# Performance work log

Hardware: AMD Instinct MI355X
Metric: run time of the kernel (lower is better)

## Reference

```python
import jax, jax.numpy as jnp
import numpy as np
import math
from jax import lax

B, T, D, K, H, MLP_DIM, WIN = 4, 2048, 1024, 64, 4, 4096, 128
KH = K // H          # eigenstates per head
HD = D // H          # attention head dim


def layer_norm(x, g, b, eps=1e-5):
    mu = jnp.mean(x, axis=-1, keepdims=True)
    var = jnp.mean(jnp.square(x - mu), axis=-1, keepdims=True)
    return (x - mu) * lax.rsqrt(var + eps) * g + b


def setup_inputs() -> dict:
    key = jax.random.key(0)
    ks = jax.random.split(key, 16)
    s = 0.02
    # layer_idx=1, n_layers=6 -> depth_ratio=0.2, decay_center=-1.7
    return {
        "x": jax.random.normal(ks[0], (B, T, D), jnp.float32),
        "prev_eigenstates": jax.random.normal(ks[1], (B, T, 2 * K), jnp.float32),
        "norm1_g": jnp.ones((D,), jnp.float32),
        "norm1_b": jnp.zeros((D,), jnp.float32),
        "in_proj_w": jax.random.normal(ks[2], (2 * K, D), jnp.float32) * s,
        "memory_gate": jnp.array(-3.0, jnp.float32),
        "memory_proj_w": jnp.eye(2 * K, dtype=jnp.float32),
        "log_decay": jax.random.uniform(ks[3], (K,), jnp.float32, -2.7, -1.2),
        "frequency": jnp.linspace(0.0, 2 * math.pi * (1 - 1 / K), K, dtype=jnp.float32),
        "coupling": jnp.tile(jnp.eye(KH, dtype=jnp.float32), (H, 1, 1))
                    + 0.01 * jax.random.normal(ks[4], (H, KH, KH), jnp.float32) / math.sqrt(KH),
        "main_gate_w": jax.random.normal(ks[5], (D, D), jnp.float32) * s,
        "main_gate_b": jnp.full((D,), -2.0, jnp.float32),
        "out_proj_w": jax.random.normal(ks[6], (D, 2 * K), jnp.float32) * s,
        "attn_norm_g": jnp.ones((D,), jnp.float32),
        "attn_norm_b": jnp.zeros((D,), jnp.float32),
        "attn_in_w": jax.random.normal(ks[7], (3 * D, D), jnp.float32) * s,
        "attn_in_b": jnp.zeros((3 * D,), jnp.float32),
        "attn_out_w": jax.random.normal(ks[8], (D, D), jnp.float32) * s,
        "attn_out_b": jnp.zeros((D,), jnp.float32),
        "norm2_g": jnp.ones((D,), jnp.float32),
        "norm2_b": jnp.zeros((D,), jnp.float32),
        "mlp_w1": jax.random.normal(ks[9], (MLP_DIM, D), jnp.float32) * s,
        "mlp_b1": jnp.zeros((MLP_DIM,), jnp.float32),
        "mlp_w2": jax.random.normal(ks[10], (D, MLP_DIM), jnp.float32) * s,
        "mlp_b2": jnp.zeros((D,), jnp.float32),
    }


def eigenstate_fft(log_decay, frequency, beta_r, beta_i):
    # diagonal complex SSM recurrence: c_t = lam * c_{t-1} + beta_t
    lam = jnp.exp(log_decay)
    lr = lam * jnp.cos(frequency)   # (K,)
    li = lam * jnp.sin(frequency)
    br = jnp.transpose(beta_r, (1, 0, 2))  # (T,B,K)
    bi = jnp.transpose(beta_i, (1, 0, 2))

    def step(carry, inp):
        sr, si = carry
        xr, xi = inp
        nr = lr * sr - li * si + xr
        ni = lr * si + li * sr + xi
        return (nr, ni), (nr, ni)

    init = (jnp.zeros(br.shape[1:], br.dtype), jnp.zeros(bi.shape[1:], bi.dtype))
    _, (cr, ci) = lax.scan(step, init, (br, bi))
    return jnp.transpose(cr, (1, 0, 2)), jnp.transpose(ci, (1, 0, 2))


def reference(x, prev_eigenstates, norm1_g, norm1_b, in_proj_w, memory_gate,
              memory_proj_w, log_decay, frequency, coupling, main_gate_w,
              main_gate_b, out_proj_w, attn_norm_g, attn_norm_b, attn_in_w,
              attn_in_b, attn_out_w, attn_out_b, norm2_g, norm2_b,
              mlp_w1, mlp_b1, mlp_w2, mlp_b2):
    b, t, d = x.shape
    residual = x
    x_norm = layer_norm(x, norm1_g, norm1_b)

    beta = jnp.einsum('btd,kd->btk', x_norm, in_proj_w)        # (B,T,2K)
    beta_r, beta_i = jnp.split(beta, 2, axis=-1)

    # cross-layer memory
    mg = jax.nn.sigmoid(memory_gate)
    prev = jnp.einsum('btk,jk->btj', prev_eigenstates, memory_proj_w)
    pr, pi = jnp.split(prev, 2, axis=-1)
    beta_r = beta_r + mg * pr
    beta_i = beta_i + mg * pi

    c_r, c_i = eigenstate_fft(log_decay, frequency, beta_r, beta_i)  # (B,T,K)

    # per-head coupling
    c_r_h = c_r.reshape(b, t, H, KH)
    c_i_h = c_i.reshape(b, t, H, KH)
    c_r = jnp.einsum('hjk,bthk->bthj', coupling, c_r_h).reshape(b, t, K)
    c_i = jnp.einsum('hjk,bthk->bthj', coupling, c_i_h).reshape(b, t, K)
    eigenstates_out = jnp.concatenate([c_r, c_i], axis=-1)     # (B,T,2K)

    h = jnp.einsum('btk,dk->btd', eigenstates_out, out_proj_w)
    # spectral gate (band gates computed in torch are unused in the output)
    main_g = jax.nn.sigmoid(jnp.einsum('btd,ed->bte', x_norm, main_gate_w) + main_gate_b)
    h = main_g * h
    x = residual + h

    # sliding-window attention (dense masked MHA, as in the source)
    attn_in = layer_norm(x, attn_norm_g, attn_norm_b)
    qkv = jnp.einsum('btd,ed->bte', attn_in, attn_in_w) + attn_in_b
    q, k_, v = jnp.split(qkv, 3, axis=-1)
    q = q.reshape(b, t, H, HD).transpose(0, 2, 1, 3)           # (B,H,T,hd)
    k_ = k_.reshape(b, t, H, HD).transpose(0, 2, 1, 3)
    v = v.reshape(b, t, H, HD).transpose(0, 2, 1, 3)
    scale = 1.0 / math.sqrt(HD)
    scores = jnp.einsum('bhqd,bhkd->bhqk', q, k_) * scale
    idx = jnp.arange(t)
    diff = idx[:, None] - idx[None, :]
    allowed = (diff >= 0) & (diff <= WIN)                      # True = attend
    scores = jnp.where(allowed, scores, jnp.finfo(scores.dtype).min)
    attn = jax.nn.softmax(scores, axis=-1)
    ao = jnp.einsum('bhqk,bhkd->bhqd', attn, v)
    ao = ao.transpose(0, 2, 1, 3).reshape(b, t, d)
    ao = jnp.einsum('btd,ed->bte', ao, attn_out_w) + attn_out_b
    x = x + ao

    # MLP
    x2 = layer_norm(x, norm2_g, norm2_b)
    m = jax.nn.silu(jnp.einsum('btd,md->btm', x2, mlp_w1) + mlp_b1)
    m = jnp.einsum('btm,dm->btd', m, mlp_w2) + mlp_b2
    x = x + m
    return (x, eigenstates_out)
```

## Files before the change

kernel.cpp:

```cpp
#include <hip/hip_runtime.h>


typedef __bf16 bf16_t;
typedef bf16_t bf16x8 __attribute__((ext_vector_type(8)));
typedef bf16_t bf16x4 __attribute__((ext_vector_type(4)));
typedef float  f32x4  __attribute__((ext_vector_type(4)));

#define Tc   2048
#define Dc   1024
#define BTc  8192
#define K2c  128
#define MLPc 4096

struct ConvSeg { const float* src; bf16_t* dst; int n; };
struct ConvArgs { ConvSeg s[9]; };

__global__ __launch_bounds__(256) void convert_kernel(ConvArgs a) {
    ConvSeg sg = a.s[blockIdx.y];
    int i = (blockIdx.x * 256 + threadIdx.x) * 4;
    if (i >= sg.n) return;
    float4 v = *(const float4*)(sg.src + i);
    bf16x4 o;
    o[0] = (bf16_t)v.x; o[1] = (bf16_t)v.y; o[2] = (bf16_t)v.z; o[3] = (bf16_t)v.w;
    *(bf16x4*)(sg.dst + i) = o;
}

__global__ __launch_bounds__(256) void ln_kernel(const float* __restrict__ x,
                                                 const float* __restrict__ g,
                                                 const float* __restrict__ bb,
                                                 bf16_t* __restrict__ out) {
    int row = blockIdx.x;
    int tid = threadIdx.x;
    float4 v = ((const float4*)(x + (size_t)row * Dc))[tid];
    float s  = v.x + v.y + v.z + v.w;
    float ss = v.x * v.x + v.y * v.y + v.z * v.z + v.w * v.w;
#pragma unroll
    for (int d = 32; d > 0; d >>= 1) {
        s  += __shfl_down(s, d);
        ss += __shfl_down(ss, d);
    }
    __shared__ float red[8];
    int wv = tid >> 6;
    if ((tid & 63) == 0) { red[wv] = s; red[4 + wv] = ss; }
    __syncthreads();
    s  = red[0] + red[1] + red[2] + red[3];
    ss = red[4] + red[5] + red[6] + red[7];
    float mean = s * (1.0f / Dc);
    float var  = ss * (1.0f / Dc) - mean * mean;
    float rstd = rsqrtf(var + 1e-5f);
    float4 g4 = ((const float4*)g)[tid];
    float4 b4 = ((const float4*)bb)[tid];
    bf16x4 o;
    o[0] = (bf16_t)((v.x - mean) * rstd * g4.x + b4.x);
    o[1] = (bf16_t)((v.y - mean) * rstd * g4.y + b4.y);
    o[2] = (bf16_t)((v.z - mean) * rstd * g4.z + b4.z);
    o[3] = (bf16_t)((v.w - mean) * rstd * g4.w + b4.w);
    *(bf16x4*)(out + (size_t)row * Dc + tid * 4) = o;
}

#define BM 128
#define BN 128
#define BKT 64

struct EpiParams {
    const float* bias;
    float*       fout;
    const float* fin;
    bf16_t*      bout;
    bf16_t*      q; bf16_t* k; bf16_t* v;
    const bf16_t* a2; const bf16_t* w2;
};

#define GLOAD_LDS(g, l)                                                        \
    __builtin_amdgcn_global_load_lds(                                          \
        (const __attribute__((address_space(1))) unsigned int*)(g),            \
        (__attribute__((address_space(3))) unsigned int*)(l), 16, 0, 0)

template <int EPI>
__global__ __launch_bounds__(256) void gemm_tiled(const bf16_t* __restrict__ A,
                                                  const bf16_t* __restrict__ W,
                                                  int M, int N, int K,
                                                  EpiParams ep) {
    __shared__ bf16_t As[BM * BKT];
    __shared__ bf16_t Bs[BN * BKT];

    int tid = threadIdx.x;
    int wv = tid >> 6, lane = tid & 63;
    int lane16 = lane & 15, quad = lane >> 4;
    int nbn = N / BN, nbm = M / BM;

    int bid = blockIdx.x;
    int xcd = bid & 7;
    int slot = bid >> 3;
    int bm_per = nbm >> 3;
    int bmo = slot / nbn;
    int bno = slot % nbn;
    if (bmo & 1) bno = nbn - 1 - bno;
    int bm = xcd * bm_per + bmo, bn = bno;
    int m0 = bm * BM, n0 = bn * BN;
    int wm = (wv >> 1) * 64, wn = (wv & 1) * 64;

    int lrow = lane >> 3;
    int lcol = ((lane & 7) ^ lrow) * 8;
    const bf16_t* ga = A + (size_t)(m0 + wv * 32 + lrow) * K + lcol;
    const bf16_t* gb = W + (size_t)(n0 + wv * 32 + lrow) * K + lcol;

    f32x4 zz = {0.f, 0.f, 0.f, 0.f};
    f32x4 acc[4][4];
#pragma unroll
    for (int mi = 0; mi < 4; mi++)
#pragma unroll
        for (int ni = 0; ni < 4; ni++) acc[mi][ni] = zz;

    for (int k0 = 0; k0 < K; k0 += BKT) {
#pragma unroll
        for (int j = 0; j < 4; j++) {
            GLOAD_LDS(ga + k0 + (size_t)(j * 8) * K, &As[(wv * 32 + j * 8) * BKT]);
            GLOAD_LDS(gb + k0 + (size_t)(j * 8) * K, &Bs[(wv * 32 + j * 8) * BKT]);
        }
        __syncthreads();
#pragma unroll
        for (int ks = 0; ks < 2; ks++) {
            bf16x8 af[4], bfr[4];
#pragma unroll
            for (int mi = 0; mi < 4; mi++)
                af[mi] = *(const bf16x8*)&As[(wm + mi * 16 + lane16) * BKT +
                                             (((ks * 4 + quad) ^ (lane16 & 7)) * 8)];
#pragma unroll
            for (int ni = 0; ni < 4; ni++)
                bfr[ni] = *(const bf16x8*)&Bs[(wn + ni * 16 + lane16) * BKT +
                                              (((ks * 4 + quad) ^ (lane16 & 7)) * 8)];
#pragma unroll
            for (int mi = 0; mi < 4; mi++)
#pragma unroll
                for (int ni = 0; ni < 4; ni++)
                    acc[mi][ni] = __builtin_amdgcn_mfma_f32_16x16x32_bf16(
                        af[mi], bfr[ni], acc[mi][ni], 0, 0, 0);
        }
        __syncthreads();
    }

    f32x4 acc2[4][4];
    if constexpr (EPI == 6) {
#pragma unroll
        for (int mi = 0; mi < 4; mi++)
#pragma unroll
            for (int ni = 0; ni < 4; ni++) acc2[mi][ni] = zz;
        const bf16_t* ga2 = ep.a2 + (size_t)(m0 + wv * 32 + lrow) * K2c + lcol;
        const bf16_t* gb2 = ep.w2 + (size_t)(n0 + wv * 32 + lrow) * K2c + lcol;
        for (int k0 = 0; k0 < K2c; k0 += BKT) {
#pragma unroll
            for (int j = 0; j < 4; j++) {
                GLOAD_LDS(ga2 + k0 + (size_t)(j * 8) * K2c, &As[(wv * 32 + j * 8) * BKT]);
                GLOAD_LDS(gb2 + k0 + (size_t)(j * 8) * K2c, &Bs[(wv * 32 + j * 8) * BKT]);
            }
            __syncthreads();
#pragma unroll
            for (int ks = 0; ks < 2; ks++) {
                bf16x8 af[4], bfr[4];
#pragma unroll
                for (int mi = 0; mi < 4; mi++)
                    af[mi] = *(const bf16x8*)&As[(wm + mi * 16 + lane16) * BKT +
                                                 (((ks * 4 + quad) ^ (lane16 & 7)) * 8)];
#pragma unroll
                for (int ni = 0; ni < 4; ni++)
                    bfr[ni] = *(const bf16x8*)&Bs[(wn + ni * 16 + lane16) * BKT +
                                                  (((ks * 4 + quad) ^ (lane16 & 7)) * 8)];
#pragma unroll
                for (int mi = 0; mi < 4; mi++)
#pragma unroll
                    for (int ni = 0; ni < 4; ni++)
                        acc2[mi][ni] = __builtin_amdgcn_mfma_f32_16x16x32_bf16(
                            af[mi], bfr[ni], acc2[mi][ni], 0, 0, 0);
            }
            __syncthreads();
        }
    }

#pragma unroll
    for (int mi = 0; mi < 4; mi++)
#pragma unroll
        for (int ni = 0; ni < 4; ni++)
#pragma unroll
            for (int r = 0; r < 4; r++) {
                int row = m0 + wm + mi * 16 + quad * 4 + r;
                int col = n0 + wn + ni * 16 + lane16;
                float v = acc[mi][ni][r];
                if constexpr (EPI == 1) {
                    v += ep.bias[col];
                    ep.bout[(size_t)row * N + col] = (bf16_t)(v / (1.0f + __expf(-v)));
                } else if constexpr (EPI == 2) {
                    size_t o = (size_t)row * N + col;
                    ep.fout[o] = ep.fin[o] + v + ep.bias[col];
                } else if constexpr (EPI == 3) {
                    v += ep.bias[col];
                    int part = col >> 10, d1 = col & 1023;
                    int hh = d1 >> 8, hd = d1 & 255;
                    int b = row >> 11, t = row & 2047;
                    bf16_t* dst = (part == 0) ? ep.q : ep.k;
                    dst[(((size_t)(b * 4 + hh) * Tc + t) << 8) + hd] = (bf16_t)v;
                } else if constexpr (EPI == 5) {
                    v += ep.bias[2048 + row];
                    int b = col >> 11, t = col & 2047;
                    int hh = row >> 8, dd = row & 255;
                    ep.v[((size_t)((b * 4 + hh) * 256 + dd)) * Tc + t] = (bf16_t)v;
                } else if constexpr (EPI == 6) {
                    size_t o = (size_t)row * N + col;
                    float g = 1.0f / (1.0f + __expf(-(v + ep.bias[col])));
                    ep.fout[o] = ep.fin[o] + g * acc2[mi][ni][r];
                }
            }
}

__device__ __forceinline__ void mm32(const bf16_t* __restrict__ A,
                                     const bf16_t* __restrict__ W,
                                     int K, int m0, int n0,
                                     int lane16, int quad, f32x4 (&acc)[2][2]) {
    const bf16_t* a0 = A + (size_t)(m0 + lane16) * K + quad * 8;
    const bf16_t* a1 = a0 + (size_t)16 * K;
    const bf16_t* w0 = W + (size_t)(n0 + lane16) * K + quad * 8;
    const bf16_t* w1 = w0 + (size_t)16 * K;
#pragma unroll 4
    for (int k = 0; k < K; k += 32) {
        bf16x8 av0 = *(const bf16x8*)(a0 + k);
        bf16x8 av1 = *(const bf16x8*)(a1 + k);
        bf16x8 bv0 = *(const bf16x8*)(w0 + k);
        bf16x8 bv1 = *(const bf16x8*)(w1 + k);
        acc[0][0] = __builtin_amdgcn_mfma_f32_16x16x32_bf16(av0, bv0, acc[0][0], 0, 0, 0);
        acc[0][1] = __builtin_amdgcn_mfma_f32_16x16x32_bf16(av0, bv1, acc[0][1], 0, 0, 0);
        acc[1][0] = __builtin_amdgcn_mfma_f32_16x16x32_bf16(av1, bv0, acc[1][0], 0, 0, 0);
        acc[1][1] = __builtin_amdgcn_mfma_f32_16x16x32_bf16(av1, bv1, acc[1][1], 0, 0, 0);
    }
}

__global__ __launch_bounds__(256) void gemm_beta(const bf16_t* __restrict__ xn,
                                                 const bf16_t* __restrict__ ipw,
                                                 const bf16_t* __restrict__ prevb,
                                                 const bf16_t* __restrict__ mpw,
                                                 const float* __restrict__ mgate_p,
                                                 float* __restrict__ beta_c) {
    int lane = threadIdx.x & 63;
    int wave = threadIdx.x >> 6;
    int gid  = blockIdx.x * 4 + wave;
    int mt = gid / 4, nt = gid % 4;
    int m0 = mt * 32, n0 = nt * 32;
    int lane16 = lane & 15, quad = lane >> 4;
    f32x4 zz = {0.f, 0.f, 0.f, 0.f};
    f32x4 acc[2][2] = {{zz, zz}, {zz, zz}};
    mm32(xn, ipw, Dc, m0, n0, lane16, quad, acc);
    f32x4 acc2[2][2] = {{zz, zz}, {zz, zz}};
    mm32(prevb, mpw, K2c, m0, n0, lane16, quad, acc2);
    float mg = 1.0f / (1.0f + __expf(-mgate_p[0]));
    for (int mi = 0; mi < 2; mi++)
        for (int ni = 0; ni < 2; ni++)
            for (int r = 0; r < 4; r++) {
                int row = m0 + mi * 16 + quad * 4 + r;
                int col = n0 + ni * 16 + lane16;
                int b = row >> 11, t = row & 2047;
                beta_c[((size_t)b * K2c + col) * Tc + t] =
                    acc[mi][ni][r] + mg * acc2[mi][ni][r];
            }
}

__global__ __launch_bounds__(64) void scan_kernel(const float* __restrict__ beta_c,
                                                  const float* __restrict__ log_decay,
                                                  const float* __restrict__ freq,
                                                  float* __restrict__ cbuf) {
    int b = blockIdx.x >> 6;
    int k = blockIdx.x & 63;
    int lane = threadIdx.x;
    float lam = expf(log_decay[k]);
    float fr = freq[k];
    float lr = lam * cosf(fr), li = lam * sinf(fr);

    const float* br_p = beta_c + ((size_t)b * K2c + k) * Tc + lane * 32;
    const float* bi_p = beta_c + ((size_t)b * K2c + 64 + k) * Tc + lane * 32;
    float br[32], bi[32];
#pragma unroll
    for (int i = 0; i < 8; i++) {
        *(float4*)(&br[i * 4]) = ((const float4*)br_p)[i];
        *(float4*)(&bi[i * 4]) = ((const float4*)bi_p)[i];
    }
    float sr = 0.f, si = 0.f;
#pragma unroll
    for (int i = 0; i < 32; i++) {
        float nr = lr * sr - li * si + br[i];
        float ni = lr * si + li * sr + bi[i];
        sr = nr; si = ni;
    }
    float Mr = lr, Mi = li;
#pragma unroll
    for (int i = 0; i < 5; i++) {
        float nr = Mr * Mr - Mi * Mi, ni = 2.f * Mr * Mi;
        Mr = nr; Mi = ni;
    }
    float ir = sr, ii = si;
#pragma unroll
    for (int d = 1; d < 64; d <<= 1) {
        float pr = __shfl_up(ir, d);
        float pi = __shfl_up(ii, d);
        if (lane >= d) {
            ir += Mr * pr - Mi * pi;
            ii += Mr * pi + Mi * pr;
        }
        float nr = Mr * Mr - Mi * Mi, ni = 2.f * Mr * Mi;
        Mr = nr; Mi = ni;
    }
    float cr = __shfl_up(ir, 1), ci = __shfl_up(ii, 1);
    if (lane == 0) { cr = 0.f; ci = 0.f; }
    float* cr_p = cbuf + ((size_t)b * K2c + k) * Tc + lane * 32;
    float* ci_p = cbuf + ((size_t)b * K2c + 64 + k) * Tc + lane * 32;
    sr = cr; si = ci;
#pragma unroll
    for (int i = 0; i < 32; i++) {
        float nr = lr * sr - li * si + br[i];
        float ni = lr * si + li * sr + bi[i];
        sr = nr; si = ni;
        cr_p[i] = sr; ci_p[i] = si;
    }
}

__global__ __launch_bounds__(256) void coupling_kernel(const float* __restrict__ cbuf,
                                                       const float* __restrict__ cpl,
                                                       float* __restrict__ eig_out,
                                                       bf16_t* __restrict__ eigb) {
    int idx = blockIdx.x * 256 + threadIdx.x;
    int col = idx & 127;
    int t = (idx >> 7) & 2047;
    int b = idx >> 18;
    int ri = col >> 6, hj = col & 63, h2 = hj >> 4, j = hj & 15;
    const float* crow = cbuf + ((size_t)b * K2c + ri * 64 + h2 * 16) * Tc + t;
    const float* cw = cpl + (h2 * 16 + j) * 16;
    float acc = 0.f;
#pragma unroll
    for (int kk = 0; kk < 16; kk++) acc += cw[kk] * crow[(size_t)kk * Tc];
    eig_out[idx] = acc;
    eigb[idx] = (bf16_t)acc;
}

#define LDP 168

__global__ __launch_bounds__(256) void attn_mfma(const bf16_t* __restrict__ qb,
                                                 const bf16_t* __restrict__ kb,
                                                 const bf16_t* __restrict__ vt,
                                                 bf16_t* __restrict__ ao) {
    __shared__ bf16_t Pl[4 * 16 * LDP];
    int tid = threadIdx.x;
    int wv = tid >> 6, lane = tid & 63;
    int lane16 = lane & 15, quad = lane >> 4;
    int qblk = blockIdx.x & 31;
    int bh = blockIdx.x >> 5;
    int qw0 = qblk * 64 + wv * 16;
    const bf16_t* qp = qb + (size_t)bh * Tc * 256;
    const bf16_t* kp = kb + (size_t)bh * Tc * 256;
    const bf16_t* vp = vt + (size_t)bh * 256 * Tc;
    bf16_t* Pw = &Pl[wv * 16 * LDP];

    for (int i = lane; i < 16 * 24; i += 64) {
        int r = i / 24, c = 144 + (i % 24);
        Pw[r * LDP + c] = (bf16_t)0.f;
    }

    bf16x8 qf[8];
#pragma unroll
    for (int ks = 0; ks < 8; ks++)
        qf[ks] = *(const bf16x8*)(qp + (size_t)(qw0 + lane16) * 256 + ks * 32 + quad * 8);

    f32x4 zz = {0.f, 0.f, 0.f, 0.f};
    f32x4 S[9];
#pragma unroll
    for (int jt = 0; jt < 9; jt++) S[jt] = zz;
    int kbase = qw0 - 128;

#pragma unroll
    for (int ks = 0; ks < 8; ks++) {
        bf16x8 kf[9];
#pragma unroll
        for (int jt = 0; jt < 9; jt++) {
            int krow = kbase + jt * 16 + lane16;
            krow = krow < 0 ? 0 : krow;
            kf[jt] = *(const bf16x8*)(kp + (size_t)krow * 256 + ks * 32 + quad * 8);
        }
#pragma unroll
        for (int jt = 0; jt < 9; jt++)
            S[jt] = __builtin_amdgcn_mfma_f32_16x16x32_bf16(qf[ks], kf[jt], S[jt], 0, 0, 0);
    }

    float m[4], l[4];
#pragma unroll
    for (int r = 0; r < 4; r++) m[r] = -1e30f;
#pragma unroll
    for (int jt = 0; jt < 9; jt++) {
        int kg = kbase + jt * 16 + lane16;
#pragma unroll
        for (int r = 0; r < 4; r++) {
            int qrow = qw0 + quad * 4 + r;
            bool ok = (kg >= 0) && (kg <= qrow) && (kg >= qrow - 128);
            float v = ok ? S[jt][r] * 0.0625f : -1e30f;
            S[jt][r] = v;
            m[r] = fmaxf(m[r], v);
        }
    }
#pragma unroll
    for (int d = 1; d < 16; d <<= 1)
#pragma unroll
        for (int r = 0; r < 4; r++)
            m[r] = fmaxf(m[r], __shfl_xor(m[r], d));
#pragma unroll
    for (int r = 0; r < 4; r++) l[r] = 0.f;
#pragma unroll
    for (int jt = 0; jt < 9; jt++)
#pragma unroll
        for (int r = 0; r < 4; r++) {
            float p = __expf(S[jt][r] - m[r]);
            S[jt][r] = p;
            l[r] += p;
        }
#pragma unroll
    for (int d = 1; d < 16; d <<= 1)
#pragma unroll
        for (int r = 0; r < 4; r++)
            l[r] += __shfl_xor(l[r], d);

#pragma unroll
    for (int jt = 0; jt < 9; jt++)
#pragma unroll
        for (int r = 0; r < 4; r++)
            Pw[(quad * 4 + r) * LDP + jt * 16 + lane16] = (bf16_t)S[jt][r];
    __syncthreads();

    f32x4 O[16];
#pragma unroll
    for (int nt = 0; nt < 16; nt++) O[nt] = zz;
#pragma unroll
    for (int ks = 0; ks < 5; ks++) {
        bf16x8 pf = *(const bf16x8*)&Pw[lane16 * LDP + ks * 32 + quad * 8];
        int kidx = kbase + ks * 32 + quad * 8;
        kidx = kidx < 0 ? 0 : kidx;
        kidx = kidx > (Tc - 8) ? (Tc - 8) : kidx;
#pragma unroll
        for (int nt = 0; nt < 16; nt++) {
            bf16x8 vf = *(const bf16x8*)(vp + (size_t)(nt * 16 + lane16) * Tc + kidx);
            O[nt] = __builtin_amdgcn_mfma_f32_16x16x32_bf16(pf, vf, O[nt], 0, 0, 0);
        }
    }

    float rl[4];
#pragma unroll
    for (int r = 0; r < 4; r++) rl[r] = 1.0f / l[r];
    int b = bh >> 2, h = bh & 3;
#pragma unroll
    for (int nt = 0; nt < 16; nt++)
#pragma unroll
        for (int r = 0; r < 4; r++) {
            int qrow = qw0 + quad * 4 + r;
            int dim = nt * 16 + lane16;
            ao[((size_t)(b * Tc + qrow)) * Dc + h * 256 + dim] = (bf16_t)(O[nt][r] * rl[r]);
        }
}

extern "C" void kernel_launch(void* const* d_in, const int* in_sizes, int n_in,
                              void* d_out, int out_size, void* d_ws, size_t ws_size,
                              hipStream_t stream) {
    const float* x            = (const float*)d_in[0];
    const float* prev_eig     = (const float*)d_in[1];
    const float* norm1_g      = (const float*)d_in[2];
    const float* norm1_b      = (const float*)d_in[3];
    const float* in_proj_w    = (const float*)d_in[4];
    const float* memory_gate  = (const float*)d_in[5];
    const float* memory_proj_w= (const float*)d_in[6];
    const float* log_decay    = (const float*)d_in[7];
    const float* frequency    = (const float*)d_in[8];
    const float* coupling     = (const float*)d_in[9];
    const float* main_gate_w  = (const float*)d_in[10];
    const float* main_gate_b  = (const float*)d_in[11];
    const float* out_proj_w   = (const float*)d_in[12];
    const float* attn_norm_g  = (const float*)d_in[13];
    const float* attn_norm_b  = (const float*)d_in[14];
    const float* attn_in_w    = (const float*)d_in[15];
    const float* attn_in_b    = (const float*)d_in[16];
    const float* attn_out_w   = (const float*)d_in[17];
    const float* attn_out_b   = (const float*)d_in[18];
    const float* norm2_g      = (const float*)d_in[19];
    const float* norm2_b      = (const float*)d_in[20];
    const float* mlp_w1       = (const float*)d_in[21];
    const float* mlp_b1       = (const float*)d_in[22];
    const float* mlp_w2       = (const float*)d_in[23];
    const float* mlp_b2       = (const float*)d_in[24];

    char* ws = (char*)d_ws;
    bf16_t* ipw_b  = (bf16_t*)(ws + 0);
    bf16_t* mpw_b  = (bf16_t*)(ws + 262144);
    bf16_t* mgw_b  = (bf16_t*)(ws + 294912);
    bf16_t* opw_b  = (bf16_t*)(ws + 2392064);
    bf16_t* aiw_b  = (bf16_t*)(ws + 2654208);
    bf16_t* aow_b  = (bf16_t*)(ws + 8945664);
    bf16_t* w1_b   = (bf16_t*)(ws + 11042816);
    bf16_t* w2_b   = (bf16_t*)(ws + 19431424);
    bf16_t* prev_b = (bf16_t*)(ws + 27820032);
    const size_t OFF_ACTA = 29917184;
    const size_t OFF_BIG  = OFF_ACTA + 16777216;
    bf16_t* actA   = (bf16_t*)(ws + OFF_ACTA);
    float*  beta_c = (float*)(ws + OFF_BIG);
    float*  cbuf   = (float*)(ws + OFF_BIG + 4194304);
    bf16_t* eigb   = (bf16_t*)(ws + OFF_BIG + 8388608);
    bf16_t* qbuf   = (bf16_t*)(ws + OFF_BIG);
    bf16_t* kbuf   = (bf16_t*)(ws + OFF_BIG + 16777216);
    bf16_t* vtbuf  = (bf16_t*)(ws + OFF_BIG + 33554432);
    bf16_t* mbuf   = (bf16_t*)(ws + OFF_BIG);

    float* out_x   = (float*)d_out;
    float* out_eig = out_x + (size_t)BTc * Dc;
    float* xres    = out_x;

    ConvArgs ca;
    ca.s[0] = ConvSeg{in_proj_w,     ipw_b,  131072};
    ca.s[1] = ConvSeg{memory_proj_w, mpw_b,  16384};
    ca.s[2] = ConvSeg{main_gate_w,   mgw_b,  1048576};
    ca.s[3] = ConvSeg{out_proj_w,    opw_b,  131072};
    ca.s[4] = ConvSeg{attn_in_w,     aiw_b,  3145728};
    ca.s[5] = ConvSeg{attn_out_w,    aow_b,  1048576};
    ca.s[6] = ConvSeg{mlp_w1,        w1_b,   4194304};
    ca.s[7] = ConvSeg{mlp_w2,        w2_b,   4194304};
    ca.s[8] = ConvSeg{prev_eig,      prev_b, 1048576};
    convert_kernel<<<dim3(4096, 9), 256, 0, stream>>>(ca);

    EpiParams ep{};

    ln_kernel<<<BTc, 256, 0, stream>>>(x, norm1_g, norm1_b, actA);
    gemm_beta<<<256, 256, 0, stream>>>(actA, ipw_b, prev_b, mpw_b, memory_gate, beta_c);
    scan_kernel<<<256, 64, 0, stream>>>(beta_c, log_decay, frequency, cbuf);
    coupling_kernel<<<4096, 256, 0, stream>>>(cbuf, coupling, out_eig, eigb);
    ep = EpiParams{}; ep.bias = main_gate_b; ep.fin = x; ep.fout = xres;
    ep.a2 = eigb; ep.w2 = opw_b;
    gemm_tiled<6><<<(BTc/BM)*(Dc/BN), 256, 0, stream>>>(actA, mgw_b, BTc, Dc, Dc, ep);
    ln_kernel<<<BTc, 256, 0, stream>>>(xres, attn_norm_g, attn_norm_b, actA);
    ep = EpiParams{}; ep.bias = attn_in_b; ep.q = qbuf; ep.k = kbuf;
    gemm_tiled<3><<<(BTc/BM)*(2048/BN), 256, 0, stream>>>(actA, aiw_b, BTc, 2048, Dc, ep);
    ep = EpiParams{}; ep.bias = attn_in_b; ep.v = vtbuf;
    gemm_tiled<5><<<(Dc/BM)*(BTc/BN), 256, 0, stream>>>(aiw_b + (size_t)2048 * Dc, actA,
                                                        Dc, BTc, Dc, ep);
    attn_mfma<<<512, 256, 0, stream>>>(qbuf, kbuf, vtbuf, actA);
    ep = EpiParams{}; ep.bias = attn_out_b; ep.fin = xres; ep.fout = xres;
    gemm_tiled<2><<<(BTc/BM)*(Dc/BN), 256, 0, stream>>>(actA, aow_b, BTc, Dc, Dc, ep);
    ln_kernel<<<BTc, 256, 0, stream>>>(xres, norm2_g, norm2_b, actA);
    ep = EpiParams{}; ep.bias = mlp_b1; ep.bout = mbuf;
    gemm_tiled<1><<<(BTc/BM)*(MLPc/BN), 256, 0, stream>>>(actA, w1_b, BTc, MLPc, Dc, ep);
    ep = EpiParams{}; ep.bias = mlp_b2; ep.fin = xres; ep.fout = out_x;
    gemm_tiled<2><<<(BTc/BM)*(Dc/BN), 256, 0, stream>>>(mbuf, w2_b, BTc, Dc, MLPc, ep);

    (void)in_sizes; (void)n_in; (void)out_size; (void)ws_size;
}
```

Baseline: 640.7 us.

## Pre-shuffle weights into MFMA fragment layout and load B operand directly from global

Weights are converted into a k8-major layout where each lane's 8-element MFMA fragment is contiguous, so GEMMs read B fragments straight from global/L2 into registers and skip the LDS staging for B. This removes half the LDS traffic and the B-side global-to-LDS loads per K step. In exchange, B fragments are fetched redundantly per wave from global memory with no LDS reuse, which relies on L2/cache bandwidth, and the shuffle conversion kernel does strided reads.

Result: slower. 660.6 us (+3.1%).

```diff
diff --git a/kernel.cpp b/kernel.cpp
--- a/kernel.cpp
+++ b/kernel.cpp
@@ -12,10 +12,12 @@
 #define K2c  128
 #define MLPc 4096
 
-struct ConvSeg { const float* src; bf16_t* dst; int n; };
-struct ConvArgs { ConvSeg s[9]; };
-
-__global__ __launch_bounds__(256) void convert_kernel(ConvArgs a) {
+struct ConvSeg  { const float* src; bf16_t* dst; int n; };
+struct ConvArgs { ConvSeg s[4]; };
+struct ShufSeg  { const float* src; bf16_t* dst; int chunks; int N; int K; };
+struct ShufArgs { ShufSeg s[6]; };
+
+__global__ __launch_bounds__(256) void convert_flat(ConvArgs a) {
     ConvSeg sg = a.s[blockIdx.y];
     int i = (blockIdx.x * 256 + threadIdx.x) * 4;
     if (i >= sg.n) return;
@@ -23,6 +25,21 @@
     bf16x4 o;
     o[0] = (bf16_t)v.x; o[1] = (bf16_t)v.y; o[2] = (bf16_t)v.z; o[3] = (bf16_t)v.w;
     *(bf16x4*)(sg.dst + i) = o;
+}
+
+__global__ __launch_bounds__(256) void convert_shuf(ShufArgs a) {
+    ShufSeg sg = a.s[blockIdx.y];
+    int idx = blockIdx.x * 256 + threadIdx.x;
+    if (idx >= sg.chunks) return;
+    int k8 = idx / sg.N;
+    int n  = idx - k8 * sg.N;
+    const float* sp = sg.src + (size_t)n * sg.K + k8 * 8;
+    float4 v0 = *(const float4*)(sp);
+    float4 v1 = *(const float4*)(sp + 4);
+    bf16x8 o;
+    o[0] = (bf16_t)v0.x; o[1] = (bf16_t)v0.y; o[2] = (bf16_t)v0.z; o[3] = (bf16_t)v0.w;
+    o[4] = (bf16_t)v1.x; o[5] = (bf16_t)v1.y; o[6] = (bf16_t)v1.z; o[7] = (bf16_t)v1.w;
+    *(bf16x8*)(sg.dst + (size_t)idx * 8) = o;
 }
 
 __global__ __launch_bounds__(256) void ln_kernel(const float* __restrict__ x,
@@ -76,13 +93,13 @@
         (const __attribute__((address_space(1))) unsigned int*)(g),            \
         (__attribute__((address_space(3))) unsigned int*)(l), 16, 0, 0)
 
-template <int EPI>
+template <int EPI, bool BDIR>
 __global__ __launch_bounds__(256) void gemm_tiled(const bf16_t* __restrict__ A,
                                                   const bf16_t* __restrict__ W,
                                                   int M, int N, int K,
                                                   EpiParams ep) {
     __shared__ bf16_t As[BM * BKT];
-    __shared__ bf16_t Bs[BN * BKT];
+    __shared__ bf16_t Bs[BDIR ? 64 : BN * BKT];
 
     int tid = threadIdx.x;
     int wv = tid >> 6, lane = tid & 63;
@@ -103,7 +120,7 @@
     int lrow = lane >> 3;
     int lcol = ((lane & 7) ^ lrow) * 8;
     const bf16_t* ga = A + (size_t)(m0 + wv * 32 + lrow) * K + lcol;
-    const bf16_t* gb = W + (size_t)(n0 + wv * 32 + lrow) * K + lcol;
+    const bf16_t* gb = BDIR ? nullptr : (W + (size_t)(n0 + wv * 32 + lrow) * K + lcol);
 
     f32x4 zz = {0.f, 0.f, 0.f, 0.f};
     f32x4 acc[4][4];
@@ -112,30 +129,44 @@
 #pragma unroll
         for (int ni = 0; ni < 4; ni++) acc[mi][ni] = zz;
 
+    int cn = n0 + wn + lane16;
+
     for (int k0 = 0; k0 < K; k0 += BKT) {
 #pragma unroll
         for (int j = 0; j < 4; j++) {
             GLOAD_LDS(ga + k0 + (size_t)(j * 8) * K, &As[(wv * 32 + j * 8) * BKT]);
-            GLOAD_LDS(gb + k0 + (size_t)(j * 8) * K, &Bs[(wv * 32 + j * 8) * BKT]);
+            if constexpr (!BDIR)
+                GLOAD_LDS(gb + k0 + (size_t)(j * 8) * K, &Bs[(wv * 32 + j * 8) * BKT]);
+        }
+        bf16x8 bfr[2][4];
+        if constexpr (BDIR) {
+#pragma unroll
+            for (int ks = 0; ks < 2; ks++)
+#pragma unroll
+                for (int ni = 0; ni < 4; ni++)
+                    bfr[ks][ni] = *(const bf16x8*)(W +
+                        ((size_t)((k0 >> 3) + ks * 4 + quad) * N + cn + ni * 16) * 8);
         }
         __syncthreads();
 #pragma unroll
         for (int ks = 0; ks < 2; ks++) {
-            bf16x8 af[4], bfr[4];
+            bf16x8 af[4];
 #pragma unroll
             for (int mi = 0; mi < 4; mi++)
                 af[mi] = *(const bf16x8*)&As[(wm + mi * 16 + lane16) * BKT +
                                              (((ks * 4 + quad) ^ (lane16 & 7)) * 8)];
-#pragma unroll
-            for (int ni = 0; ni < 4; ni++)
-                bfr[ni] = *(const bf16x8*)&Bs[(wn + ni * 16 + lane16) * BKT +
-                                              (((ks * 4 + quad) ^ (lane16 & 7)) * 8)];
+            if constexpr (!BDIR) {
+#pragma unroll
+                for (int ni = 0; ni < 4; ni++)
+                    bfr[ks][ni] = *(const bf16x8*)&Bs[(wn + ni * 16 + lane16) * BKT +
+                                                  (((ks * 4 + quad) ^ (lane16 & 7)) * 8)];
+            }
 #pragma unroll
             for (int mi = 0; mi < 4; mi++)
 #pragma unroll
                 for (int ni = 0; ni < 4; ni++)
                     acc[mi][ni] = __builtin_amdgcn_mfma_f32_16x16x32_bf16(
-                        af[mi], bfr[ni], acc[mi][ni], 0, 0, 0);
+                        af[mi], bfr[ks][ni], acc[mi][ni], 0, 0, 0);
         }
         __syncthreads();
     }
@@ -147,31 +178,31 @@
 #pragma unroll
             for (int ni = 0; ni < 4; ni++) acc2[mi][ni] = zz;
         const bf16_t* ga2 = ep.a2 + (size_t)(m0 + wv * 32 + lrow) * K2c + lcol;
-        const bf16_t* gb2 = ep.w2 + (size_t)(n0 + wv * 32 + lrow) * K2c + lcol;
         for (int k0 = 0; k0 < K2c; k0 += BKT) {
 #pragma unroll
-            for (int j = 0; j < 4; j++) {
+            for (int j = 0; j < 4; j++)
                 GLOAD_LDS(ga2 + k0 + (size_t)(j * 8) * K2c, &As[(wv * 32 + j * 8) * BKT]);
-                GLOAD_LDS(gb2 + k0 + (size_t)(j * 8) * K2c, &Bs[(wv * 32 + j * 8) * BKT]);
-            }
+            bf16x8 bfr[2][4];
+#pragma unroll
+            for (int ks = 0; ks < 2; ks++)
+#pragma unroll
+                for (int ni = 0; ni < 4; ni++)
+                    bfr[ks][ni] = *(const bf16x8*)(ep.w2 +
+                        ((size_t)((k0 >> 3) + ks * 4 + quad) * N + cn + ni * 16) * 8);
             __syncthreads();
 #pragma unroll
             for (int ks = 0; ks < 2; ks++) {
-                bf16x8 af[4], bfr[4];
+                bf16x8 af[4];
 #pragma unroll
                 for (int mi = 0; mi < 4; mi++)
                     af[mi] = *(const bf16x8*)&As[(wm + mi * 16 + lane16) * BKT +
                                                  (((ks * 4 + quad) ^ (lane16 & 7)) * 8)];
 #pragma unroll
-                for (int ni = 0; ni < 4; ni++)
-                    bfr[ni] = *(const bf16x8*)&Bs[(wn + ni * 16 + lane16) * BKT +
-                                                  (((ks * 4 + quad) ^ (lane16 & 7)) * 8)];
-#pragma unroll
                 for (int mi = 0; mi < 4; mi++)
 #pragma unroll
                     for (int ni = 0; ni < 4; ni++)
                         acc2[mi][ni] = __builtin_amdgcn_mfma_f32_16x16x32_bf16(
-                            af[mi], bfr[ni], acc2[mi][ni], 0, 0, 0);
+                            af[mi], bfr[ks][ni], acc2[mi][ni], 0, 0, 0);
             }
             __syncthreads();
         }
@@ -489,15 +520,16 @@
     const float* mlp_b2       = (const float*)d_in[24];
 
     char* ws = (char*)d_ws;
-    bf16_t* ipw_b  = (bf16_t*)(ws + 0);
-    bf16_t* mpw_b  = (bf16_t*)(ws + 262144);
-    bf16_t* mgw_b  = (bf16_t*)(ws + 294912);
-    bf16_t* opw_b  = (bf16_t*)(ws + 2392064);
-    bf16_t* aiw_b  = (bf16_t*)(ws + 2654208);
-    bf16_t* aow_b  = (bf16_t*)(ws + 8945664);
-    bf16_t* w1_b   = (bf16_t*)(ws + 11042816);
-    bf16_t* w2_b   = (bf16_t*)(ws + 19431424);
-    bf16_t* prev_b = (bf16_t*)(ws + 27820032);
+    bf16_t* ipw_b   = (bf16_t*)(ws + 0);
+    bf16_t* mpw_b   = (bf16_t*)(ws + 262144);
+    bf16_t* mgw_s   = (bf16_t*)(ws + 294912);
+    bf16_t* opw_s   = (bf16_t*)(ws + 2392064);
+    bf16_t* aiw_s   = (bf16_t*)(ws + 2654208);
+    bf16_t* aiwv_b  = (bf16_t*)(ws + 2654208 + 4194304);
+    bf16_t* aow_s   = (bf16_t*)(ws + 8945664);
+    bf16_t* w1_s    = (bf16_t*)(ws + 11042816);
+    bf16_t* w2_s    = (bf16_t*)(ws + 19431424);
+    bf16_t* prev_b  = (bf16_t*)(ws + 27820032);
     const size_t OFF_ACTA = 29917184;
     const size_t OFF_BIG  = OFF_ACTA + 16777216;
     bf16_t* actA   = (bf16_t*)(ws + OFF_ACTA);
@@ -514,16 +546,20 @@
     float* xres    = out_x;
 
     ConvArgs ca;
-    ca.s[0] = ConvSeg{in_proj_w,     ipw_b,  131072};
-    ca.s[1] = ConvSeg{memory_proj_w, mpw_b,  16384};
-    ca.s[2] = ConvSeg{main_gate_w,   mgw_b,  1048576};
-    ca.s[3] = ConvSeg{out_proj_w,    opw_b,  131072};
-    ca.s[4] = ConvSeg{attn_in_w,     aiw_b,  3145728};
-    ca.s[5] = ConvSeg{attn_out_w,    aow_b,  1048576};
-    ca.s[6] = ConvSeg{mlp_w1,        w1_b,   4194304};
-    ca.s[7] = ConvSeg{mlp_w2,        w2_b,   4194304};
-    ca.s[8] = ConvSeg{prev_eig,      prev_b, 1048576};
-    convert_kernel<<<dim3(4096, 9), 256, 0, stream>>>(ca);
+    ca.s[0] = ConvSeg{in_proj_w,           ipw_b,  131072};
+    ca.s[1] = ConvSeg{memory_proj_w,       mpw_b,  16384};
+    ca.s[2] = ConvSeg{prev_eig,            prev_b, 1048576};
+    ca.s[3] = ConvSeg{attn_in_w + (size_t)2048 * Dc, aiwv_b, 1048576};
+    convert_flat<<<dim3(1024, 4), 256, 0, stream>>>(ca);
+
+    ShufArgs sa;
+    sa.s[0] = ShufSeg{main_gate_w, mgw_s, 131072, 1024, 1024};
+    sa.s[1] = ShufSeg{out_proj_w,  opw_s, 16384,  1024, 128};
+    sa.s[2] = ShufSeg{attn_in_w,   aiw_s, 262144, 2048, 1024};
+    sa.s[3] = ShufSeg{attn_out_w,  aow_s, 131072, 1024, 1024};
+    sa.s[4] = ShufSeg{mlp_w1,      w1_s,  524288, 4096, 1024};
+    sa.s[5] = ShufSeg{mlp_w2,      w2_s,  524288, 1024, 4096};
+    convert_shuf<<<dim3(2048, 6), 256, 0, stream>>>(sa);
 
     EpiParams ep{};
 
@@ -532,22 +568,21 @@
     scan_kernel<<<256, 64, 0, stream>>>(beta_c, log_decay, frequency, cbuf);
     coupling_kernel<<<4096, 256, 0, stream>>>(cbuf, coupling, out_eig, eigb);
     ep = EpiParams{}; ep.bias = main_gate_b; ep.fin = x; ep.fout = xres;
-    ep.a2 = eigb; ep.w2 = opw_b;
-    gemm_tiled<6><<<(BTc/BM)*(Dc/BN), 256, 0, stream>>>(actA, mgw_b, BTc, Dc, Dc, ep);
+    ep.a2 = eigb; ep.w2 = opw_s;
+    gemm_tiled<6, true><<<(BTc/BM)*(Dc/BN), 256, 0, stream>>>(actA, mgw_s, BTc, Dc, Dc, ep);
     ln_kernel<<<BTc, 256, 0, stream>>>(xres, attn_norm_g, attn_norm_b, actA);
     ep = EpiParams{}; ep.bias = attn_in_b; ep.q = qbuf; ep.k = kbuf;
-    gemm_tiled<3><<<(BTc/BM)*(2048/BN), 256, 0, stream>>>(actA, aiw_b, BTc, 2048, Dc, ep);
+    gemm_tiled<3, true><<<(BTc/BM)*(2048/BN), 256, 0, stream>>>(actA, aiw_s, BTc, 2048, Dc, ep);
     ep = EpiParams{}; ep.bias = attn_in_b; ep.v = vtbuf;
-    gemm_tiled<5><<<(Dc/BM)*(BTc/BN), 256, 0, stream>>>(aiw_b + (size_t)2048 * Dc, actA,
-                                                        Dc, BTc, Dc, ep);
+    gemm_tiled<5, false><<<(Dc/BM)*(BTc/BN), 256, 0, stream>>>(aiwv_b, actA, Dc, BTc, Dc, ep);
     attn_mfma<<<512, 256, 0, stream>>>(qbuf, kbuf, vtbuf, actA);
     ep = EpiParams{}; ep.bias = attn_out_b; ep.fin = xres; ep.fout = xres;
-    gemm_tiled<2><<<(BTc/BM)*(Dc/BN), 256, 0, stream>>>(actA, aow_b, BTc, Dc, Dc, ep);
+    gemm_tiled<2, true><<<(BTc/BM)*(Dc/BN), 256, 0, stream>>>(actA, aow_s, BTc, Dc, Dc, ep);
     ln_kernel<<<BTc, 256, 0, stream>>>(xres, norm2_g, norm2_b, actA);
     ep = EpiParams{}; ep.bias = mlp_b1; ep.bout = mbuf;
-    gemm_tiled<1><<<(BTc/BM)*(MLPc/BN), 256, 0, stream>>>(actA, w1_b, BTc, MLPc, Dc, ep);
+    gemm_tiled<1, true><<<(BTc/BM)*(MLPc/BN), 256, 0, stream>>>(actA, w1_s, BTc, MLPc, Dc, ep);
     ep = EpiParams{}; ep.bias = mlp_b2; ep.fin = xres; ep.fout = out_x;
-    gemm_tiled<2><<<(BTc/BM)*(Dc/BN), 256, 0, stream>>>(mbuf, w2_b, BTc, Dc, MLPc, ep);
+    gemm_tiled<2, true><<<(BTc/BM)*(Dc/BN), 256, 0, stream>>>(mbuf, w2_s, BTc, Dc, MLPc, ep);
 
     (void)in_sizes; (void)n_in; (void)out_size; (void)ws_size;
 }
```
